# Kernel optimization log

Hardware: AMD Instinct MI355X
Metric: run time of the kernel (lower is better)

The kernel has to match this reference:

```python
import jax, jax.numpy as jnp
import numpy as np

N = 50000      # nodes
E = 800000     # edges
F_IN = 128     # input_dim
H = 4          # GAT heads
C = 32         # hidden_dim (per head)
HC = H * C     # 128, concat GAT output
NG = 64        # graphs in batch
OUT = 10       # classes


def _gat_conv(x, src, dst, W, att_src, att_dst, bias):
    # PyG GATConv (concat=True, add_self_loops=True, negative_slope=0.2)
    n = x.shape[0]
    h = (x @ W).reshape(n, H, -1)                      # [N,H,C]
    a_s = (h * att_src).sum(-1)                        # [N,H]
    a_d = (h * att_dst).sum(-1)                        # [N,H]
    loop = jnp.arange(n)
    s = jnp.concatenate([src, loop])                   # self-loops appended
    d = jnp.concatenate([dst, loop])
    e = jax.nn.leaky_relu(a_s[s] + a_d[d], 0.2)        # [E+N,H]
    m = jax.ops.segment_max(e, d, num_segments=n)
    e = jnp.exp(e - m[d])
    z = jax.ops.segment_sum(e, d, num_segments=n)
    alpha = e / (z[d] + 1e-16)                         # edge softmax per dst,head
    out = jax.ops.segment_sum(h[s] * alpha[..., None], d, num_segments=n)
    return out.reshape(n, -1) + bias                   # [N,H*C]


def setup_inputs() -> dict:
    key = jax.random.key(0)
    ks = jax.random.split(key, 20)
    g = lambda k, shp, fan: jax.random.normal(k, shp, jnp.float32) / np.sqrt(fan)
    inp = {
        'x': jax.random.normal(ks[0], (N, F_IN), jnp.float32),
        'edge_index': jax.random.randint(ks[1], (2, E), 0, N),
        'batch': jnp.sort(jax.random.randint(ks[2], (N,), 0, NG)),
        # GATConv 1: F_IN -> H*C
        'W1': g(ks[3], (F_IN, HC), F_IN),
        'as1': g(ks[4], (H, C), C), 'ad1': g(ks[5], (H, C), C),
        'b1': jnp.zeros((HC,), jnp.float32),
        # GATConv 2: H*C -> H*C
        'W2': g(ks[6], (HC, HC), HC),
        'as2': g(ks[7], (H, C), C), 'ad2': g(ks[8], (H, C), C),
        'b2': jnp.zeros((HC,), jnp.float32),
        # GraphConv: H*C -> C  (lin_rel has bias, lin_root does not)
        'W3r': g(ks[9], (HC, C), HC), 'W3l': g(ks[10], (HC, C), HC),
        'b3': jnp.zeros((C,), jnp.float32),
        # SAGEConv: C -> C (mean aggr; lin_l has bias, lin_r does not)
        'W4l': g(ks[11], (C, C), C), 'b4l': jnp.zeros((C,), jnp.float32),
        'W4r': g(ks[12], (C, C), C),
        # MLP head
        'Wf1': g(ks[13], (C, C), C), 'bf1': jnp.zeros((C,), jnp.float32),
        'Wf2': g(ks[14], (C, OUT), C), 'bf2': jnp.zeros((OUT,), jnp.float32),
    }
    return inp


def reference(x, edge_index, batch, W1, as1, ad1, b1, W2, as2, ad2, b2,
              W3r, W3l, b3, W4l, b4l, W4r, Wf1, bf1, Wf2, bf2):
    src, dst = edge_index[0], edge_index[1]
    relu = jax.nn.relu
    n = x.shape[0]
    # GAT layers (dropout is identity in eval)
    x = relu(_gat_conv(x, src, dst, W1, as1, ad1, b1))
    x = relu(_gat_conv(x, src, dst, W2, as2, ad2, b2))
    # GraphConv: lin_rel(sum_neighbors) + lin_root(x)
    agg = jax.ops.segment_sum(x[src], dst, num_segments=n)
    x = relu(agg @ W3r + b3 + x @ W3l)
    # SAGEConv: lin_l(mean_neighbors) + lin_r(x)
    deg = jax.ops.segment_sum(jnp.ones((src.shape[0],), x.dtype), dst, num_segments=n)
    mean = jax.ops.segment_sum(x[src], dst, num_segments=n) / jnp.maximum(deg, 1.0)[:, None]
    x = relu(mean @ W4l + b4l + x @ W4r)
    # global mean pool over graphs
    cnt = jax.ops.segment_sum(jnp.ones((n,), x.dtype), batch, num_segments=NG)
    gpool = jax.ops.segment_sum(x, batch, num_segments=NG) / jnp.maximum(cnt, 1.0)[:, None]
    gpool = relu(gpool @ Wf1 + bf1)
    return gpool @ Wf2 + bf2
```

## Files before the change

### kernel.cpp

```cpp
#include <hip/hip_runtime.h>
#include <hip/hip_bf16.h>
#include <type_traits>


typedef __bf16 v8bf __attribute__((ext_vector_type(8)));
typedef float  v4f  __attribute__((ext_vector_type(4)));

__device__ __forceinline__ float lrelu(float x) { return x > 0.f ? x : 0.2f * x; }

__device__ __forceinline__ unsigned short f2bf(float f) {
    unsigned u = __float_as_uint(f);
    unsigned r = (u + 0x7FFF + ((u >> 16) & 1)) >> 16;
    return (unsigned short)r;
}
__device__ __forceinline__ float bfbits2f(unsigned short u) {
    return __uint_as_float((unsigned)u << 16);
}
__device__ __forceinline__ float bflo(int v) { return __uint_as_float((unsigned)v << 16); }
__device__ __forceinline__ float bfhi(int v) { return __uint_as_float((unsigned)v & 0xffff0000u); }
__device__ __forceinline__ int packbf2(float a, float b) {
    return (int)f2bf(a) | ((int)f2bf(b) << 16);
}


__global__ __launch_bounds__(256) void bucket_hist(const int* __restrict__ dst,
                                                   int* __restrict__ bcount,
                                                   int E, int nbuck) {
    __shared__ int hist[256];
    int t = threadIdx.x;
    for (int i = t; i < nbuck; i += 256) hist[i] = 0;
    __syncthreads();
    int base = blockIdx.x * 4096;
    #pragma unroll
    for (int k = 0; k < 16; ++k) {
        int e = base + k * 256 + t;
        if (e < E) atomicAdd(&hist[dst[e] >> 8], 1);
    }
    __syncthreads();
    for (int i = t; i < nbuck; i += 256) {
        int c = hist[i];
        if (c) atomicAdd(&bcount[i], c);
    }
}

__global__ __launch_bounds__(256) void scan_convert(
    const int* __restrict__ bcount, int* __restrict__ bbase, int* __restrict__ gcursor,
    int nbuck, int E, int* __restrict__ rowptr, int n,
    const float* __restrict__ W1, const float* __restrict__ W2,
    const float* __restrict__ W3r, const float* __restrict__ W3l,
    const float* __restrict__ as1, const float* __restrict__ ad1,
    const float* __restrict__ as2, const float* __restrict__ ad2,
    __hip_bfloat16* __restrict__ W1t, __hip_bfloat16* __restrict__ W2t,
    __hip_bfloat16* __restrict__ W3rt, __hip_bfloat16* __restrict__ W3lt)
{
    int t = threadIdx.x;
    if (blockIdx.x == 0) {
        __shared__ int red[256];
        int v = (t < nbuck) ? bcount[t] : 0;
        red[t] = v;
        __syncthreads();
        for (int off = 1; off < 256; off <<= 1) {
            int u = (t >= off) ? red[t - off] : 0;
            __syncthreads();
            red[t] += u;
            __syncthreads();
        }
        int ex = red[t] - v;
        if (t < nbuck) { bbase[t] = ex; gcursor[t] = ex; }
        if (t == 0) { bbase[nbuck] = E; rowptr[n] = E; }
        return;
    }
    int b = blockIdx.x - 1;
    int i = b * 256 + t;
    {
        int k = i >> 7, c = i & 127;
        *(unsigned short*)&W1t[c * 128 + k] = f2bf(W1[i]);
        *(unsigned short*)&W2t[c * 128 + k] = f2bf(W2[i]);
    }
    if (i < 4096) {
        int k = i >> 5, c = i & 31;
        *(unsigned short*)&W3rt[c * 128 + k] = f2bf(W3r[i]);
        *(unsigned short*)&W3lt[c * 128 + k] = f2bf(W3l[i]);
    }
    if (b == 0) {
        for (int u = t; u < 512; u += 256) {
            int k = u & 127, hd = u >> 7;
            float vs1 = 0.f, vd1 = 0.f, vs2 = 0.f, vd2 = 0.f;
            #pragma unroll
            for (int j = 0; j < 32; ++j) {
                int c = hd * 32 + j;
                float w1 = W1[k * 128 + c], w2 = W2[k * 128 + c];
                vs1 += w1 * as1[c]; vd1 += w1 * ad1[c];
                vs2 += w2 * as2[c]; vd2 += w2 * ad2[c];
            }
            unsigned short h1s = f2bf(vs1), h1d = f2bf(vd1);
            unsigned short h2s = f2bf(vs2), h2d = f2bf(vd2);
            *(unsigned short*)&W1t[(128 + hd) * 128 + k] = h1s;
            *(unsigned short*)&W1t[(132 + hd) * 128 + k] = f2bf(vs1 - bfbits2f(h1s));
            *(unsigned short*)&W1t[(136 + hd) * 128 + k] = h1d;
            *(unsigned short*)&W1t[(140 + hd) * 128 + k] = f2bf(vd1 - bfbits2f(h1d));
            *(unsigned short*)&W2t[(128 + hd) * 128 + k] = h2s;
            *(unsigned short*)&W2t[(132 + hd) * 128 + k] = f2bf(vs2 - bfbits2f(h2s));
            *(unsigned short*)&W2t[(136 + hd) * 128 + k] = h2d;
            *(unsigned short*)&W2t[(140 + hd) * 128 + k] = f2bf(vd2 - bfbits2f(h2d));
        }
    }
}

__global__ __launch_bounds__(256) void bucket_scatter(const int* __restrict__ dst,
                                                      const int* __restrict__ src,
                                                      int* __restrict__ gcursor,
                                                      int* __restrict__ pairs,
                                                      int E, int nbuck) {
    __shared__ int hist[256], lcur[256];
    int t = threadIdx.x;
    for (int i = t; i < nbuck; i += 256) hist[i] = 0;
    __syncthreads();
    int base = blockIdx.x * 2048;
    int dreg[8];
    #pragma unroll
    for (int k = 0; k < 8; ++k) {
        int e = base + k * 256 + t;
        int d = (e < E) ? dst[e] : -1;
        dreg[k] = d;
        if (d >= 0) atomicAdd(&hist[d >> 8], 1);
    }
    __syncthreads();
    for (int i = t; i < nbuck; i += 256) {
        int c = hist[i];
        lcur[i] = c ? atomicAdd(&gcursor[i], c) : 0;
    }
    __syncthreads();
    #pragma unroll
    for (int k = 0; k < 8; ++k) {
        int e = base + k * 256 + t;
        if (e < E) {
            int d = dreg[k];
            int p = atomicAdd(&lcur[d >> 8], 1);
            pairs[p] = ((d & 255) << 17) | src[e];
        }
    }
}

__global__ __launch_bounds__(256) void bucket_fill(const int* __restrict__ pairs,
                                                   const int* __restrict__ bbase,
                                                   int* __restrict__ rowptr,
                                                   int* __restrict__ colsrc, int n) {
    __shared__ int deg[256], excl[256], cur[256];
    int b = blockIdx.x, t = threadIdx.x;
    int e0 = bbase[b], e1 = bbase[b + 1];
    int d0 = b << 8;
    deg[t] = 0;
    __syncthreads();
    for (int j = e0 + t; j < e1; j += 256)
        atomicAdd(&deg[pairs[j] >> 17], 1);
    __syncthreads();
    int v = deg[t];
    excl[t] = v;
    __syncthreads();
    for (int off = 1; off < 256; off <<= 1) {
        int u = (t >= off) ? excl[t - off] : 0;
        __syncthreads();
        excl[t] += u;
        __syncthreads();
    }
    int base = e0 + excl[t] - v;
    if (d0 + t < n) rowptr[d0 + t] = base;
    cur[t] = base;
    __syncthreads();
    for (int j = e0 + t; j < e1; j += 256) {
        int w = pairs[j];
        int p = atomicAdd(&cur[w >> 17], 1);
        colsrc[p] = w & 0x1FFFF;
    }
}

template <typename T>
__global__ __launch_bounds__(256) void gemm_att_mfma(
    const T* __restrict__ X, const __hip_bfloat16* __restrict__ Wt,
    __hip_bfloat16* __restrict__ h, float* __restrict__ a_s, float* __restrict__ a_d, int n)
{
    __shared__ __align__(16) __hip_bfloat16 sWt[144 * 136];
    int t = threadIdx.x;
    for (int i = t; i < 144 * 16; i += 256) {
        int row = i >> 4, ch = i & 15;
        *(int4*)&sWt[row * 136 + ch * 8] = *(const int4*)&Wt[row * 128 + ch * 8];
    }
    __syncthreads();
    int wave = t >> 6, lane = t & 63, quad = lane >> 4, l16 = lane & 15;
    int rowbase = (blockIdx.x * 4 + wave) * 16;
    if (rowbase >= n) return;

    v8bf z;
    #pragma unroll
    for (int i = 0; i < 8; ++i) z[i] = (__bf16)0.f;
    int arow = rowbase + l16;
    bool ok = arow < n;
    v8bf af[4];
    if constexpr (std::is_same<T, float>::value) {
        const float* xf = X + (size_t)(ok ? arow : 0) * 128;
        #pragma unroll
        for (int ks = 0; ks < 4; ++ks) {
            if (ok) {
                float4 u = *(const float4*)&xf[ks * 32 + quad * 8];
                float4 v = *(const float4*)&xf[ks * 32 + quad * 8 + 4];
                v8bf a;
                unsigned short r;
                r = f2bf(u.x); a[0] = *(__bf16*)&r;
                r = f2bf(u.y); a[1] = *(__bf16*)&r;
                r = f2bf(u.z); a[2] = *(__bf16*)&r;
                r = f2bf(u.w); a[3] = *(__bf16*)&r;
                r = f2bf(v.x); a[4] = *(__bf16*)&r;
                r = f2bf(v.y); a[5] = *(__bf16*)&r;
                r = f2bf(v.z); a[6] = *(__bf16*)&r;
                r = f2bf(v.w); a[7] = *(__bf16*)&r;
                af[ks] = a;
            } else af[ks] = z;
        }
    } else {
        const v8bf* px = (const v8bf*)(X + (size_t)(ok ? arow : 0) * 128);
        #pragma unroll
        for (int ks = 0; ks < 4; ++ks) af[ks] = ok ? px[ks * 4 + quad] : z;
    }

    v4f acc[9];
    #pragma unroll
    for (int ct = 0; ct < 9; ++ct) acc[ct] = (v4f){0.f, 0.f, 0.f, 0.f};
    #pragma unroll
    for (int ct = 0; ct < 9; ++ct) {
        #pragma unroll
        for (int ks = 0; ks < 4; ++ks) {
            v8bf b = *(const v8bf*)&sWt[(ct * 16 + l16) * 136 + ks * 32 + quad * 8];
            acc[ct] = __builtin_amdgcn_mfma_f32_16x16x32_bf16(af[ks], b, acc[ct], 0, 0, 0);
        }
    }

    #pragma unroll
    for (int reg = 0; reg < 4; ++reg) {
        int r = rowbase + quad * 4 + reg;
        if (r < n) {
            #pragma unroll
            for (int ct = 0; ct < 8; ++ct)
                *(unsigned short*)&h[(size_t)r * 128 + ct * 16 + l16] = f2bf(acc[ct][reg]);
        }
    }
    #pragma unroll
    for (int reg = 0; reg < 4; ++reg) {
        float v = acc[8][reg] + __shfl_xor(acc[8][reg], 4);
        int r = rowbase + quad * 4 + reg;
        if (r < n) {
            if (l16 < 4)                    a_s[r * 4 + l16] = v;
            else if (l16 >= 8 && l16 < 12)  a_d[r * 4 + (l16 - 8)] = v;
        }
    }
}

__global__ __launch_bounds__(256) void gat_aggr(
    const __hip_bfloat16* __restrict__ h, const float* __restrict__ a_s,
    const float* __restrict__ a_d,
    const int* __restrict__ rowptr, const int* __restrict__ colsrc,
    const float* __restrict__ bias, __hip_bfloat16* __restrict__ out, int n)
{
    __shared__ float s_w[4][64 * 4];
    int t = threadIdx.x;
    int wave = t >> 6, lane = t & 63;
    int d = blockIdx.x * 4 + wave;
    if (d >= n) d = n - 1;
    int beg = rowptr[d], end = rowptr[d + 1];
    int cnt = end - beg;
    float4 ad4 = *(const float4*)&a_d[d * 4];
    float4 asd = *(const float4*)&a_s[d * 4];
    float es0 = lrelu(asd.x + ad4.x), es1 = lrelu(asd.y + ad4.y);
    float es2 = lrelu(asd.z + ad4.z), es3 = lrelu(asd.w + ad4.w);
    float z0 = 0.f, z1 = 0.f, z2 = 0.f, z3 = 0.f;

    int l16 = lane & 15, egrp = lane >> 4;
    int ch = l16 * 8;
    int head = l16 >> 2;
    float acc[8];
    #pragma unroll
    for (int i = 0; i < 8; ++i) acc[i] = 0.f;

    for (int j0 = 0; j0 < cnt; j0 += 64) {
        int ne = min(64, cnt - j0);
        float w0 = 0.f, w1 = 0.f, w2 = 0.f, w3 = 0.f;
        int s = 0;
        if (lane < ne) {
            s = colsrc[beg + j0 + lane];
            float4 sv = *(const float4*)&a_s[s * 4];
            w0 = __expf(lrelu(sv.x + ad4.x));
            w1 = __expf(lrelu(sv.y + ad4.y));
            w2 = __expf(lrelu(sv.z + ad4.z));
            w3 = __expf(lrelu(sv.w + ad4.w));
        }
        z0 += w0; z1 += w1; z2 += w2; z3 += w3;
        float4 wv = {w0, w1, w2, w3};
        *(float4*)&s_w[wave][lane * 4] = wv;
        __asm volatile("s_waitcnt lgkmcnt(0)" ::: "memory");
        int kmax = (ne + 3) >> 2;
        #pragma unroll 2
        for (int k = 0; k < kmax; ++k) {
            int j = egrp + 4 * k;
            int ss = __shfl(s, j);
            float wj = s_w[wave][j * 4 + head];
            int4 u = *(const int4*)&h[(size_t)ss * 128 + ch];
            acc[0] += wj * bflo(u.x); acc[1] += wj * bfhi(u.x);
            acc[2] += wj * bflo(u.y); acc[3] += wj * bfhi(u.y);
            acc[4] += wj * bflo(u.z); acc[5] += wj * bfhi(u.z);
            acc[6] += wj * bflo(u.w); acc[7] += wj * bfhi(u.w);
        }
    }
    #pragma unroll
    for (int off = 1; off < 64; off <<= 1) {
        z0 += __shfl_xor(z0, off);
        z1 += __shfl_xor(z1, off);
        z2 += __shfl_xor(z2, off);
        z3 += __shfl_xor(z3, off);
    }
    #pragma unroll
    for (int off = 16; off < 64; off <<= 1)
        #pragma unroll
        for (int i = 0; i < 8; ++i) acc[i] += __shfl_xor(acc[i], off);

    if (egrp == 0) {
        float zh = (head < 2) ? (head == 0 ? z0 : z1) : (head == 2 ? z2 : z3);
        float eh = (head < 2) ? (head == 0 ? es0 : es1) : (head == 2 ? es2 : es3);
        float ws = __expf(eh);
        float inv = 1.f / (zh + ws + 1e-16f);
        int4 hu = *(const int4*)&h[(size_t)d * 128 + ch];
        float hs[8] = {bflo(hu.x), bfhi(hu.x), bflo(hu.y), bfhi(hu.y),
                       bflo(hu.z), bfhi(hu.z), bflo(hu.w), bfhi(hu.w)};
        float4 b0 = *(const float4*)&bias[ch];
        float4 b1 = *(const float4*)&bias[ch + 4];
        float o[8];
        o[0] = fmaxf((acc[0] + ws * hs[0]) * inv + b0.x, 0.f);
        o[1] = fmaxf((acc[1] + ws * hs[1]) * inv + b0.y, 0.f);
        o[2] = fmaxf((acc[2] + ws * hs[2]) * inv + b0.z, 0.f);
        o[3] = fmaxf((acc[3] + ws * hs[3]) * inv + b0.w, 0.f);
        o[4] = fmaxf((acc[4] + ws * hs[4]) * inv + b1.x, 0.f);
        o[5] = fmaxf((acc[5] + ws * hs[5]) * inv + b1.y, 0.f);
        o[6] = fmaxf((acc[6] + ws * hs[6]) * inv + b1.z, 0.f);
        o[7] = fmaxf((acc[7] + ws * hs[7]) * inv + b1.w, 0.f);
        int4 ou;
        ou.x = packbf2(o[0], o[1]); ou.y = packbf2(o[2], o[3]);
        ou.z = packbf2(o[4], o[5]); ou.w = packbf2(o[6], o[7]);
        *(int4*)&out[(size_t)d * 128 + ch] = ou;
    }
}

__global__ __launch_bounds__(256) void graphconv_lin(
    const __hip_bfloat16* __restrict__ Xb,
    const __hip_bfloat16* __restrict__ Wrt, const __hip_bfloat16* __restrict__ Wlt,
    const float* __restrict__ bias, __hip_bfloat16* __restrict__ y,
    float* __restrict__ root, int n)
{
    __shared__ __align__(16) __hip_bfloat16 sWr[32 * 136], sWl[32 * 136];
    int t = threadIdx.x;
    for (int i = t; i < 32 * 16; i += 256) {
        int row = i >> 4, ch = i & 15;
        *(int4*)&sWr[row * 136 + ch * 8] = *(const int4*)&Wrt[row * 128 + ch * 8];
        *(int4*)&sWl[row * 136 + ch * 8] = *(const int4*)&Wlt[row * 128 + ch * 8];
    }
    __syncthreads();
    int wave = t >> 6, lane = t & 63, quad = lane >> 4, l16 = lane & 15;
    int rowbase = (blockIdx.x * 4 + wave) * 16;
    if (rowbase >= n) return;

    v8bf z;
    #pragma unroll
    for (int i = 0; i < 8; ++i) z[i] = (__bf16)0.f;
    int arow = rowbase + l16;
    bool ok = arow < n;
    const v8bf* px = (const v8bf*)(Xb + (size_t)(ok ? arow : 0) * 128);
    v8bf fx[4];
    #pragma unroll
    for (int ks = 0; ks < 4; ++ks) fx[ks] = ok ? px[ks * 4 + quad] : z;

    v4f accR[2], accL[2];
    #pragma unroll
    for (int ct = 0; ct < 2; ++ct) {
        accR[ct] = (v4f){0.f, 0.f, 0.f, 0.f};
        accL[ct] = (v4f){0.f, 0.f, 0.f, 0.f};
        #pragma unroll
        for (int ks = 0; ks < 4; ++ks) {
            v8bf br = *(const v8bf*)&sWr[(ct * 16 + l16) * 136 + ks * 32 + quad * 8];
            accR[ct] = __builtin_amdgcn_mfma_f32_16x16x32_bf16(fx[ks], br, accR[ct], 0, 0, 0);
            v8bf bl = *(const v8bf*)&sWl[(ct * 16 + l16) * 136 + ks * 32 + quad * 8];
            accL[ct] = __builtin_amdgcn_mfma_f32_16x16x32_bf16(fx[ks], bl, accL[ct], 0, 0, 0);
        }
    }
    #pragma unroll
    for (int ct = 0; ct < 2; ++ct) {
        float bcol = bias[ct * 16 + l16];
        #pragma unroll
        for (int reg = 0; reg < 4; ++reg) {
            int r = rowbase + quad * 4 + reg;
            if (r < n) {
                *(unsigned short*)&y[(size_t)r * 32 + ct * 16 + l16] = f2bf(accR[ct][reg]);
                root[(size_t)r * 32 + ct * 16 + l16] = accL[ct][reg] + bcol;
            }
        }
    }
}

__global__ __launch_bounds__(256) void graphconv_aggr(
    const __hip_bfloat16* __restrict__ y, const float* __restrict__ root,
    const int* __restrict__ rowptr, const int* __restrict__ colsrc,
    __hip_bfloat16* __restrict__ x3, int n)
{
    int t = threadIdx.x;
    int wave = t >> 6, lane = t & 63;
    int d = blockIdx.x * 4 + wave;
    if (d >= n) d = n - 1;
    int beg = rowptr[d], end = rowptr[d + 1];
    int cnt = end - beg;
    int l4 = lane & 3, egrp = lane >> 2;
    int ch = l4 * 8;
    float acc[8];
    #pragma unroll
    for (int i = 0; i < 8; ++i) acc[i] = 0.f;
    for (int j0 = 0; j0 < cnt; j0 += 64) {
        int ne = min(64, cnt - j0);
        int s = (lane < ne) ? colsrc[beg + j0 + lane] : 0;
        int kmax = (ne + 15) >> 4;
        #pragma unroll 2
        for (int k = 0; k < kmax; ++k) {
            int j = egrp + 16 * k;
            int ss = __shfl(s, j);
            float m = (j < ne) ? 1.f : 0.f;
            int4 u = *(const int4*)&y[(size_t)ss * 32 + ch];
            acc[0] += m * bflo(u.x); acc[1] += m * bfhi(u.x);
            acc[2] += m * bflo(u.y); acc[3] += m * bfhi(u.y);
            acc[4] += m * bflo(u.z); acc[5] += m * bfhi(u.z);
            acc[6] += m * bflo(u.w); acc[7] += m * bfhi(u.w);
        }
    }
    #pragma unroll
    for (int off = 4; off < 64; off <<= 1)
        #pragma unroll
        for (int i = 0; i < 8; ++i) acc[i] += __shfl_xor(acc[i], off);
    if (egrp == 0) {
        float4 r0 = *(const float4*)&root[(size_t)d * 32 + ch];
        float4 r1 = *(const float4*)&root[(size_t)d * 32 + ch + 4];
        float o[8];
        o[0] = fmaxf(acc[0] + r0.x, 0.f); o[1] = fmaxf(acc[1] + r0.y, 0.f);
        o[2] = fmaxf(acc[2] + r0.z, 0.f); o[3] = fmaxf(acc[3] + r0.w, 0.f);
        o[4] = fmaxf(acc[4] + r1.x, 0.f); o[5] = fmaxf(acc[5] + r1.y, 0.f);
        o[6] = fmaxf(acc[6] + r1.z, 0.f); o[7] = fmaxf(acc[7] + r1.w, 0.f);
        int4 ou;
        ou.x = packbf2(o[0], o[1]); ou.y = packbf2(o[2], o[3]);
        ou.z = packbf2(o[4], o[5]); ou.w = packbf2(o[6], o[7]);
        *(int4*)&x3[(size_t)d * 32 + ch] = ou;
    }
}

__global__ __launch_bounds__(256) void mean_aggr32(
    const __hip_bfloat16* __restrict__ x, const int* __restrict__ rowptr,
    const int* __restrict__ colsrc, float* __restrict__ mean, int n)
{
    int t = threadIdx.x;
    int wave = t >> 6, lane = t & 63;
    int d = blockIdx.x * 4 + wave;
    if (d >= n) d = n - 1;
    int beg = rowptr[d], end = rowptr[d + 1];
    int cnt = end - beg;
    int l4 = lane & 3, egrp = lane >> 2;
    int ch = l4 * 8;
    float acc[8];
    #pragma unroll
    for (int i = 0; i < 8; ++i) acc[i] = 0.f;
    for (int j0 = 0; j0 < cnt; j0 += 64) {
        int ne = min(64, cnt - j0);
        int s = (lane < ne) ? colsrc[beg + j0 + lane] : 0;
        int kmax = (ne + 15) >> 4;
        #pragma unroll 2
        for (int k = 0; k < kmax; ++k) {
            int j = egrp + 16 * k;
            int ss = __shfl(s, j);
            float m = (j < ne) ? 1.f : 0.f;
            int4 u = *(const int4*)&x[(size_t)ss * 32 + ch];
            acc[0] += m * bflo(u.x); acc[1] += m * bfhi(u.x);
            acc[2] += m * bflo(u.y); acc[3] += m * bfhi(u.y);
            acc[4] += m * bflo(u.z); acc[5] += m * bfhi(u.z);
            acc[6] += m * bflo(u.w); acc[7] += m * bfhi(u.w);
        }
    }
    #pragma unroll
    for (int off = 4; off < 64; off <<= 1)
        #pragma unroll
        for (int i = 0; i < 8; ++i) acc[i] += __shfl_xor(acc[i], off);
    if (egrp == 0) {
        float invd = 1.f / fmaxf((float)cnt, 1.f);
        float4 lo = {acc[0] * invd, acc[1] * invd, acc[2] * invd, acc[3] * invd};
        float4 hi = {acc[4] * invd, acc[5] * invd, acc[6] * invd, acc[7] * invd};
        *(float4*)&mean[(size_t)d * 32 + ch]     = lo;
        *(float4*)&mean[(size_t)d * 32 + ch + 4] = hi;
    }
}

__global__ __launch_bounds__(256) void sage_gemm(
    const float* __restrict__ mean, const __hip_bfloat16* __restrict__ xin,
    const float* __restrict__ Wl, const float* __restrict__ bl,
    const float* __restrict__ Wr, float* __restrict__ out, int n)
{
    __shared__ __align__(16) float sWl[32 * 32], sWr[32 * 32];
    __shared__ __align__(16) float sm[8 * 32], sx[8 * 32];
    int t = threadIdx.x;
    for (int i = t; i < 1024; i += 256) { sWl[i] = Wl[i]; sWr[i] = Wr[i]; }
    int c = t & 31, rr = t >> 5;
    float bc = bl[c];
    for (int row0 = blockIdx.x * 8; row0 < n; row0 += gridDim.x * 8) {
        __syncthreads();
        {
            int i = t;
            int r = i >> 5, cc = i & 31;
            int row = row0 + r;
            sm[i] = (row < n) ? mean[row * 32 + cc] : 0.f;
            sx[i] = (row < n) ? bfbits2f(*(const unsigned short*)&xin[row * 32 + cc]) : 0.f;
        }
        __syncthreads();
        float acc = bc;
        const float4* pm = (const float4*)&sm[rr * 32];
        const float4* px = (const float4*)&sx[rr * 32];
        #pragma unroll
        for (int k4 = 0; k4 < 8; ++k4) {
            float4 vm = pm[k4], vx = px[k4];
            const float* wl = &sWl[(k4 * 4) * 32 + c];
            const float* wr = &sWr[(k4 * 4) * 32 + c];
            acc += vm.x * wl[0] + vm.y * wl[32] + vm.z * wl[64] + vm.w * wl[96];
            acc += vx.x * wr[0] + vx.y * wr[32] + vx.z * wr[64] + vx.w * wr[96];
        }
        int row = row0 + rr;
        if (row < n) out[row * 32 + c] = fmaxf(acc, 0.f);
    }
}

__device__ __forceinline__ int lower_bound_i(const int* a, int n, int key) {
    int lo = 0, hi = n;
    while (lo < hi) { int mid = (lo + hi) >> 1; if (a[mid] < key) lo = mid + 1; else hi = mid; }
    return lo;
}

__global__ __launch_bounds__(256) void pool_kernel(
    const float* __restrict__ x, const int* __restrict__ batch,
    float* __restrict__ gpool, int n)
{
    int g = blockIdx.x;
    int lo = lower_bound_i(batch, n, g);
    int hi = lower_bound_i(batch, n, g + 1);
    int t = threadIdx.x;
    int c = t & 31, rr = t >> 5;
    float acc = 0.f;
    for (int i = lo + rr; i < hi; i += 8) acc += x[i * 32 + c];
    __shared__ float sred[256];
    sred[t] = acc;
    __syncthreads();
    if (t < 128) sred[t] += sred[t + 128];
    __syncthreads();
    if (t < 64) sred[t] += sred[t + 64];
    __syncthreads();
    if (t < 32) {
        float v = sred[t] + sred[t + 32];
        gpool[g * 32 + t] = v / fmaxf((float)(hi - lo), 1.f);
    }
}

__global__ __launch_bounds__(256) void head_kernel(
    const float* __restrict__ gpool, const float* __restrict__ Wf1, const float* __restrict__ bf1,
    const float* __restrict__ Wf2, const float* __restrict__ bf2, float* __restrict__ out)
{
    __shared__ float sg[64 * 32], st[64 * 32];
    __shared__ float sW1[32 * 32], sW2[32 * 10];
    int t = threadIdx.x;
    for (int i = t; i < 2048; i += 256) sg[i] = gpool[i];
    for (int i = t; i < 1024; i += 256) sW1[i] = Wf1[i];
    for (int i = t; i < 320; i += 256) sW2[i] = Wf2[i];
    __syncthreads();
    for (int i = t; i < 2048; i += 256) {
        int g = i >> 5, c = i & 31;
        float acc = bf1[c];
        #pragma unroll
        for (int k = 0; k < 32; ++k) acc += sg[g * 32 + k] * sW1[k * 32 + c];
        st[i] = fmaxf(acc, 0.f);
    }
    __syncthreads();
    for (int i = t; i < 640; i += 256) {
        int g = i / 10, o = i - g * 10;
        float acc = bf2[o];
        #pragma unroll
        for (int k = 0; k < 32; ++k) acc += st[g * 32 + k] * sW2[k * 10 + o];
        out[i] = acc;
    }
}

extern "C" void kernel_launch(void* const* d_in, const int* in_sizes, int n_in,
                              void* d_out, int out_size, void* d_ws, size_t ws_size,
                              hipStream_t stream) {
    const float* x    = (const float*)d_in[0];
    const int*   ei   = (const int*)d_in[1];
    const int*   batch= (const int*)d_in[2];
    const float* W1   = (const float*)d_in[3];
    const float* as1  = (const float*)d_in[4];
    const float* ad1  = (const float*)d_in[5];
    const float* b1   = (const float*)d_in[6];
    const float* W2   = (const float*)d_in[7];
    const float* as2  = (const float*)d_in[8];
    const float* ad2  = (const float*)d_in[9];
    const float* b2   = (const float*)d_in[10];
    const float* W3r  = (const float*)d_in[11];
    const float* W3l  = (const float*)d_in[12];
    const float* b3   = (const float*)d_in[13];
    const float* W4l  = (const float*)d_in[14];
    const float* b4l  = (const float*)d_in[15];
    const float* W4r  = (const float*)d_in[16];
    const float* Wf1  = (const float*)d_in[17];
    const float* bf1  = (const float*)d_in[18];
    const float* Wf2  = (const float*)d_in[19];
    const float* bf2  = (const float*)d_in[20];

    const int N = in_sizes[0] / 128;
    const int E = in_sizes[1] / 2;
    const int* src = ei;
    const int* dst = ei + E;

    char* p = (char*)d_ws;
    auto alloc = [&](size_t bytes) -> void* {
        void* r = (void*)p;
        p += (bytes + 255) & ~(size_t)255;
        return r;
    };
    __hip_bfloat16* buf1 = (__hip_bfloat16*)alloc((size_t)N * 128 * 2);
    __hip_bfloat16* buf2 = (__hip_bfloat16*)alloc((size_t)N * 128 * 2);
    __hip_bfloat16* buf3 = (__hip_bfloat16*)alloc((size_t)N * 128 * 2);
    float* aS     = (float*)alloc((size_t)N * 4 * 4);
    float* aD     = (float*)alloc((size_t)N * 4 * 4);
    int*   rowptr = (int*)alloc((size_t)(N + 1) * 4);
    int*   colsrc = (int*)alloc((size_t)E * 4);
    int*   bcount = (int*)alloc(256 * 4);
    int*   bbase  = (int*)alloc(257 * 4);
    int*   gcursor= (int*)alloc(256 * 4);
    __hip_bfloat16* W1t  = (__hip_bfloat16*)alloc(144 * 128 * 2);
    __hip_bfloat16* W2t  = (__hip_bfloat16*)alloc(144 * 128 * 2);
    __hip_bfloat16* W3rt = (__hip_bfloat16*)alloc(32 * 128 * 2);
    __hip_bfloat16* W3lt = (__hip_bfloat16*)alloc(32 * 128 * 2);
    float* gpool  = (float*)alloc(64 * 32 * 4);

    __hip_bfloat16* X3b  = buf2;
    float*          MEAN = (float*)((char*)buf2 + (((size_t)N * 32 * 2 + 255) & ~(size_t)255));
    float*          X4   = (float*)buf1;
    __hip_bfloat16* Y32  = buf3;
    float*          ROOT = (float*)((char*)buf3 + (((size_t)N * 32 * 2 + 255) & ~(size_t)255));
    int*            pairs = (int*)buf3;

    const int nbuck = (N + 255) >> 8;

    hipMemsetAsync(bcount, 0, 256 * 4, stream);
    bucket_hist<<<(E + 4095) / 4096, 256, 0, stream>>>(dst, bcount, E, nbuck);
    scan_convert<<<65, 256, 0, stream>>>(bcount, bbase, gcursor, nbuck, E, rowptr, N,
                                         W1, W2, W3r, W3l, as1, ad1, as2, ad2,
                                         W1t, W2t, W3rt, W3lt);
    bucket_scatter<<<(E + 2047) / 2048, 256, 0, stream>>>(dst, src, gcursor, pairs, E, nbuck);
    bucket_fill<<<nbuck, 256, 0, stream>>>(pairs, bbase, rowptr, colsrc, N);

    const int gmm = (N + 63) / 64;
    const int gag = (N + 3) / 4;
    gemm_att_mfma<float><<<gmm, 256, 0, stream>>>(x, W1t, buf3, aS, aD, N);
    gat_aggr<<<gag, 256, 0, stream>>>(buf3, aS, aD, rowptr, colsrc, b1, buf2, N);
    gemm_att_mfma<__hip_bfloat16><<<gmm, 256, 0, stream>>>(buf2, W2t, buf3, aS, aD, N);
    gat_aggr<<<gag, 256, 0, stream>>>(buf3, aS, aD, rowptr, colsrc, b2, buf1, N);
    graphconv_lin<<<gmm, 256, 0, stream>>>(buf1, W3rt, W3lt, b3, Y32, ROOT, N);
    graphconv_aggr<<<gag, 256, 0, stream>>>(Y32, ROOT, rowptr, colsrc, X3b, N);
    mean_aggr32<<<gag, 256, 0, stream>>>(X3b, rowptr, colsrc, MEAN, N);
    sage_gemm<<<1024, 256, 0, stream>>>(MEAN, X3b, W4l, b4l, W4r, X4, N);
    pool_kernel<<<64, 256, 0, stream>>>(X4, batch, gpool, N);
    head_kernel<<<1, 256, 0, stream>>>(gpool, Wf1, bf1, Wf2, bf2, (float*)d_out);
}
```

Baseline: 357.4 us.

## Fuse SAGE mean aggregation with its GEMM and pack aggregation FMAs

Merges the mean-aggregation kernel and the SAGE dense layer into one kernel. Each wave computes the neighbor mean for its node, stages it and the root features in LDS, and applies the two 32x32 weight matrices in place. This removes the fp32 MEAN intermediate round trip and one launch. The aggregation loops in the GAT, GraphConv and SAGE kernels now accumulate in float2 vectors so the compiler can emit packed FMAs, and compute gather addresses with 32-bit byte offsets. In exchange, every block of 12.5k reloads both weight matrices into LDS, and the 32-bit offsets assume the buffers stay under 4 GB.

```diff
diff --git a/kernel.cpp b/kernel.cpp
--- a/kernel.cpp
+++ b/kernel.cpp
@@ -5,6 +5,7 @@
 
 typedef __bf16 v8bf __attribute__((ext_vector_type(8)));
 typedef float  v4f  __attribute__((ext_vector_type(4)));
+typedef float  v2f  __attribute__((ext_vector_type(2)));
 
 __device__ __forceinline__ float lrelu(float x) { return x > 0.f ? x : 0.2f * x; }
 
@@ -18,6 +19,9 @@
 }
 __device__ __forceinline__ float bflo(int v) { return __uint_as_float((unsigned)v << 16); }
 __device__ __forceinline__ float bfhi(int v) { return __uint_as_float((unsigned)v & 0xffff0000u); }
+__device__ __forceinline__ v2f up2(int v) {
+    v2f r; r.x = bflo(v); r.y = bfhi(v); return r;
+}
 __device__ __forceinline__ int packbf2(float a, float b) {
     return (int)f2bf(a) | ((int)f2bf(b) << 16);
 }
@@ -275,11 +279,11 @@
     float z0 = 0.f, z1 = 0.f, z2 = 0.f, z3 = 0.f;
 
     int l16 = lane & 15, egrp = lane >> 4;
-    int ch = l16 * 8;
+    unsigned ch2 = (unsigned)(l16 * 16);
     int head = l16 >> 2;
-    float acc[8];
-    #pragma unroll
-    for (int i = 0; i < 8; ++i) acc[i] = 0.f;
+    v2f a2[4];
+    #pragma unroll
+    for (int i = 0; i < 4; ++i) a2[i] = (v2f){0.f, 0.f};
 
     for (int j0 = 0; j0 < cnt; j0 += 64) {
         int ne = min(64, cnt - j0);
@@ -303,13 +307,17 @@
             int j = egrp + 4 * k;
             int ss = __shfl(s, j);
             float wj = s_w[wave][j * 4 + head];
-            int4 u = *(const int4*)&h[(size_t)ss * 128 + ch];
-            acc[0] += wj * bflo(u.x); acc[1] += wj * bfhi(u.x);
-            acc[2] += wj * bflo(u.y); acc[3] += wj * bfhi(u.y);
-            acc[4] += wj * bflo(u.z); acc[5] += wj * bfhi(u.z);
-            acc[6] += wj * bflo(u.w); acc[7] += wj * bfhi(u.w);
-        }
-    }
+            v2f w2v = {wj, wj};
+            unsigned off = ((unsigned)ss << 8) + ch2;
+            int4 u = *(const int4*)((const char*)h + off);
+            a2[0] += w2v * up2(u.x);
+            a2[1] += w2v * up2(u.y);
+            a2[2] += w2v * up2(u.z);
+            a2[3] += w2v * up2(u.w);
+        }
+    }
+    float acc[8] = {a2[0].x, a2[0].y, a2[1].x, a2[1].y,
+                    a2[2].x, a2[2].y, a2[3].x, a2[3].y};
     #pragma unroll
     for (int off = 1; off < 64; off <<= 1) {
         z0 += __shfl_xor(z0, off);
@@ -323,6 +331,7 @@
         for (int i = 0; i < 8; ++i) acc[i] += __shfl_xor(acc[i], off);
 
     if (egrp == 0) {
+        int ch = l16 * 8;
         float zh = (head < 2) ? (head == 0 ? z0 : z1) : (head == 2 ? z2 : z3);
         float eh = (head < 2) ? (head == 0 ? es0 : es1) : (head == 2 ? es2 : es3);
         float ws = __expf(eh);
@@ -415,10 +424,10 @@
     int beg = rowptr[d], end = rowptr[d + 1];
     int cnt = end - beg;
     int l4 = lane & 3, egrp = lane >> 2;
-    int ch = l4 * 8;
-    float acc[8];
-    #pragma unroll
-    for (int i = 0; i < 8; ++i) acc[i] = 0.f;
+    unsigned ch2 = (unsigned)(l4 * 16);
+    v2f a2[4];
+    #pragma unroll
+    for (int i = 0; i < 4; ++i) a2[i] = (v2f){0.f, 0.f};
     for (int j0 = 0; j0 < cnt; j0 += 64) {
         int ne = min(64, cnt - j0);
         int s = (lane < ne) ? colsrc[beg + j0 + lane] : 0;
@@ -428,18 +437,23 @@
             int j = egrp + 16 * k;
             int ss = __shfl(s, j);
             float m = (j < ne) ? 1.f : 0.f;
-            int4 u = *(const int4*)&y[(size_t)ss * 32 + ch];
-            acc[0] += m * bflo(u.x); acc[1] += m * bfhi(u.x);
-            acc[2] += m * bflo(u.y); acc[3] += m * bfhi(u.y);
-            acc[4] += m * bflo(u.z); acc[5] += m * bfhi(u.z);
-            acc[6] += m * bflo(u.w); acc[7] += m * bfhi(u.w);
-        }
-    }
+            v2f m2 = {m, m};
+            unsigned off = ((unsigned)ss << 6) + ch2;
+            int4 u = *(const int4*)((const char*)y + off);
+            a2[0] += m2 * up2(u.x);
+            a2[1] += m2 * up2(u.y);
+            a2[2] += m2 * up2(u.z);
+            a2[3] += m2 * up2(u.w);
+        }
+    }
+    float acc[8] = {a2[0].x, a2[0].y, a2[1].x, a2[1].y,
+                    a2[2].x, a2[2].y, a2[3].x, a2[3].y};
     #pragma unroll
     for (int off = 4; off < 64; off <<= 1)
         #pragma unroll
         for (int i = 0; i < 8; ++i) acc[i] += __shfl_xor(acc[i], off);
     if (egrp == 0) {
+        int ch = l4 * 8;
         float4 r0 = *(const float4*)&root[(size_t)d * 32 + ch];
         float4 r1 = *(const float4*)&root[(size_t)d * 32 + ch + 4];
         float o[8];
@@ -454,21 +468,28 @@
     }
 }
 
-__global__ __launch_bounds__(256) void mean_aggr32(
-    const __hip_bfloat16* __restrict__ x, const int* __restrict__ rowptr,
-    const int* __restrict__ colsrc, float* __restrict__ mean, int n)
-{
-    int t = threadIdx.x;
+__global__ __launch_bounds__(256) void sage_fused(
+    const __hip_bfloat16* __restrict__ x3, const int* __restrict__ rowptr,
+    const int* __restrict__ colsrc,
+    const float* __restrict__ W4l, const float* __restrict__ b4l,
+    const float* __restrict__ W4r, float* __restrict__ out, int n)
+{
+    __shared__ __align__(16) float sWl[32 * 32], sWr[32 * 32];
+    __shared__ float s_mean[4][32], s_x3[4][32];
+    int t = threadIdx.x;
+    for (int i = t; i < 1024; i += 256) { sWl[i] = W4l[i]; sWr[i] = W4r[i]; }
+    __syncthreads();
+
     int wave = t >> 6, lane = t & 63;
     int d = blockIdx.x * 4 + wave;
     if (d >= n) d = n - 1;
     int beg = rowptr[d], end = rowptr[d + 1];
     int cnt = end - beg;
     int l4 = lane & 3, egrp = lane >> 2;
-    int ch = l4 * 8;
-    float acc[8];
-    #pragma unroll
-    for (int i = 0; i < 8; ++i) acc[i] = 0.f;
+    unsigned ch2 = (unsigned)(l4 * 16);
+    v2f a2[4];
+    #pragma unroll
+    for (int i = 0; i < 4; ++i) a2[i] = (v2f){0.f, 0.f};
     for (int j0 = 0; j0 < cnt; j0 += 64) {
         int ne = min(64, cnt - j0);
         int s = (lane < ne) ? colsrc[beg + j0 + lane] : 0;
@@ -478,61 +499,45 @@
             int j = egrp + 16 * k;
             int ss = __shfl(s, j);
             float m = (j < ne) ? 1.f : 0.f;
-            int4 u = *(const int4*)&x[(size_t)ss * 32 + ch];
-            acc[0] += m * bflo(u.x); acc[1] += m * bfhi(u.x);
-            acc[2] += m * bflo(u.y); acc[3] += m * bfhi(u.y);
-            acc[4] += m * bflo(u.z); acc[5] += m * bfhi(u.z);
-            acc[6] += m * bflo(u.w); acc[7] += m * bfhi(u.w);
-        }
-    }
+            v2f m2 = {m, m};
+            unsigned off = ((unsigned)ss << 6) + ch2;
+            int4 u = *(const int4*)((const char*)x3 + off);
+            a2[0] += m2 * up2(u.x);
+            a2[1] += m2 * up2(u.y);
+            a2[2] += m2 * up2(u.z);
+            a2[3] += m2 * up2(u.w);
+        }
+    }
+    float acc[8] = {a2[0].x, a2[0].y, a2[1].x, a2[1].y,
+                    a2[2].x, a2[2].y, a2[3].x, a2[3].y};
     #pragma unroll
     for (int off = 4; off < 64; off <<= 1)
         #pragma unroll
         for (int i = 0; i < 8; ++i) acc[i] += __shfl_xor(acc[i], off);
     if (egrp == 0) {
+        int ch = l4 * 8;
         float invd = 1.f / fmaxf((float)cnt, 1.f);
-        float4 lo = {acc[0] * invd, acc[1] * invd, acc[2] * invd, acc[3] * invd};
-        float4 hi = {acc[4] * invd, acc[5] * invd, acc[6] * invd, acc[7] * invd};
-        *(float4*)&mean[(size_t)d * 32 + ch]     = lo;
-        *(float4*)&mean[(size_t)d * 32 + ch + 4] = hi;
-    }
-}
-
-__global__ __launch_bounds__(256) void sage_gemm(
-    const float* __restrict__ mean, const __hip_bfloat16* __restrict__ xin,
-    const float* __restrict__ Wl, const float* __restrict__ bl,
-    const float* __restrict__ Wr, float* __restrict__ out, int n)
-{
-    __shared__ __align__(16) float sWl[32 * 32], sWr[32 * 32];
-    __shared__ __align__(16) float sm[8 * 32], sx[8 * 32];
-    int t = threadIdx.x;
-    for (int i = t; i < 1024; i += 256) { sWl[i] = Wl[i]; sWr[i] = Wr[i]; }
-    int c = t & 31, rr = t >> 5;
-    float bc = bl[c];
-    for (int row0 = blockIdx.x * 8; row0 < n; row0 += gridDim.x * 8) {
-        __syncthreads();
-        {
-            int i = t;
-            int r = i >> 5, cc = i & 31;
-            int row = row0 + r;
-            sm[i] = (row < n) ? mean[row * 32 + cc] : 0.f;
-            sx[i] = (row < n) ? bfbits2f(*(const unsigned short*)&xin[row * 32 + cc]) : 0.f;
-        }
-        __syncthreads();
-        float acc = bc;
-        const float4* pm = (const float4*)&sm[rr * 32];
-        const float4* px = (const float4*)&sx[rr * 32];
-        #pragma unroll
-        for (int k4 = 0; k4 < 8; ++k4) {
-            float4 vm = pm[k4], vx = px[k4];
-            const float* wl = &sWl[(k4 * 4) * 32 + c];
-            const float* wr = &sWr[(k4 * 4) * 32 + c];
-            acc += vm.x * wl[0] + vm.y * wl[32] + vm.z * wl[64] + vm.w * wl[96];
-            acc += vx.x * wr[0] + vx.y * wr[32] + vx.z * wr[64] + vx.w * wr[96];
-        }
-        int row = row0 + rr;
-        if (row < n) out[row * 32 + c] = fmaxf(acc, 0.f);
-    }
+        int4 xr = *(const int4*)&x3[(size_t)d * 32 + ch];
+        #pragma unroll
+        for (int i = 0; i < 8; ++i) s_mean[wave][ch + i] = acc[i] * invd;
+        s_x3[wave][ch + 0] = bflo(xr.x); s_x3[wave][ch + 1] = bfhi(xr.x);
+        s_x3[wave][ch + 2] = bflo(xr.y); s_x3[wave][ch + 3] = bfhi(xr.y);
+        s_x3[wave][ch + 4] = bflo(xr.z); s_x3[wave][ch + 5] = bfhi(xr.z);
+        s_x3[wave][ch + 6] = bflo(xr.w); s_x3[wave][ch + 7] = bfhi(xr.w);
+    }
+    __asm volatile("s_waitcnt lgkmcnt(0)" ::: "memory");
+    int c = lane & 31, half = lane >> 5;
+    const float* sm = &s_mean[wave][half * 16];
+    const float* sx = &s_x3[wave][half * 16];
+    float acc2 = 0.f;
+    #pragma unroll
+    for (int k = 0; k < 16; ++k) {
+        int kk = half * 16 + k;
+        acc2 += sm[k] * sWl[kk * 32 + c] + sx[k] * sWr[kk * 32 + c];
+    }
+    acc2 += __shfl_xor(acc2, 32);
+    if (half == 0 && d < n)
+        out[(size_t)d * 32 + c] = fmaxf(acc2 + b4l[c], 0.f);
 }
 
 __device__ __forceinline__ int lower_bound_i(const int* a, int n, int key) {
@@ -646,7 +651,6 @@
     float* gpool  = (float*)alloc(64 * 32 * 4);
 
     __hip_bfloat16* X3b  = buf2;
-    float*          MEAN = (float*)((char*)buf2 + (((size_t)N * 32 * 2 + 255) & ~(size_t)255));
     float*          X4   = (float*)buf1;
     __hip_bfloat16* Y32  = buf3;
     float*          ROOT = (float*)((char*)buf3 + (((size_t)N * 32 * 2 + 255) & ~(size_t)255));
@@ -670,8 +674,7 @@
     gat_aggr<<<gag, 256, 0, stream>>>(buf3, aS, aD, rowptr, colsrc, b2, buf1, N);
     graphconv_lin<<<gmm, 256, 0, stream>>>(buf1, W3rt, W3lt, b3, Y32, ROOT, N);
     graphconv_aggr<<<gag, 256, 0, stream>>>(Y32, ROOT, rowptr, colsrc, X3b, N);
-    mean_aggr32<<<gag, 256, 0, stream>>>(X3b, rowptr, colsrc, MEAN, N);
-    sage_gemm<<<1024, 256, 0, stream>>>(MEAN, X3b, W4l, b4l, W4r, X4, N);
+    sage_fused<<<gag, 256, 0, stream>>>(X3b, rowptr, colsrc, W4l, b4l, W4r, X4, N);
     pool_kernel<<<64, 256, 0, stream>>>(X4, batch, gpool, N);
     head_kernel<<<1, 256, 0, stream>>>(gpool, Wf1, bf1, Wf2, bf2, (float*)d_out);
 }
```

New measurement: 360.7 us. About the same (+0.9%).
